# Performance work log

Measured on AMD Instinct MI355X. Metric: run time of the kernel, lower is better.

Reference implementation:

```python
import jax, jax.numpy as jnp
import numpy as np

B, T, C, NH = 8, 1024, 1024, 16
DH = C // NH  # 64


def setup_inputs() -> dict:
    key = jax.random.key(0)
    ks = jax.random.split(key, 7)
    s = 1.0 / np.sqrt(C)
    return {
        "x": jax.random.normal(ks[0], (B, T, C), dtype=jnp.float32),
        "Wq": jax.random.normal(ks[1], (C, C), dtype=jnp.float32) * s,
        "bq": jnp.zeros((C,), dtype=jnp.float32),
        "Wk": jax.random.normal(ks[2], (C, C), dtype=jnp.float32) * s,
        "bk": jnp.zeros((C,), dtype=jnp.float32),
        "Wv": jax.random.normal(ks[3], (C, C), dtype=jnp.float32) * s,
        "bv": jnp.zeros((C,), dtype=jnp.float32),
    }


def reference(x, Wq, bq, Wk, bk, Wv, bv):
    # Linear projections (weights stored as [in, out])
    q = x @ Wq + bq  # [B, T, C]
    k = x @ Wk + bk
    v = x @ Wv + bv
    q = q.reshape(B, T, NH, DH)
    k = k.reshape(B, T, NH, DH)
    v = v.reshape(B, T, NH, DH)
    scale = 1.0 / np.sqrt(DH)
    # NOTE: source module's causal mask buffer is all-ones due to a non-inplace
    # masked_fill bug, so attention is NON-causal (mask multiply is a no-op).
    attn = jnp.einsum("bqhd,bkhd->bhqk", q, k) * scale  # [B, NH, T, T]
    attn = jax.nn.softmax(attn, axis=-1)
    # dropout is identity (p=0 / eval)
    o = jnp.einsum("bhqk,bkhd->bqhd", attn, v)  # [B, T, NH, DH]
    return o.reshape(B, T, C)
```

## Files before the change

kernel.cpp:

```cpp
#include <hip/hip_runtime.h>


#define B_  8
#define T_  1024
#define C_  1024
#define NH_ 16
#define DH_ 64
#define M_  (B_ * T_)

typedef __bf16 bf16x8 __attribute__((ext_vector_type(8)));
typedef float  floatx4 __attribute__((ext_vector_type(4)));

__device__ __forceinline__ unsigned short f2bf(float f) {
    unsigned int u = __float_as_uint(f);
    unsigned int r = (u + 0x7fffu + ((u >> 16) & 1u)) >> 16;
    return (unsigned short)r;
}

__device__ __forceinline__ unsigned int f2bf2(float a, float b) {
    unsigned int ua = __float_as_uint(a), ub = __float_as_uint(b);
    ua += 0x7fffu + ((ua >> 16) & 1u);
    ub += 0x7fffu + ((ub >> 16) & 1u);
#if __has_builtin(__builtin_amdgcn_perm)
    return __builtin_amdgcn_perm(ub, ua, 0x07060302u);
#else
    return (ua >> 16) | (ub & 0xffff0000u);
#endif
}

__device__ __forceinline__ void gload_lds16(const void* g, void* l) {
    __builtin_amdgcn_global_load_lds(
        (const __attribute__((address_space(1))) unsigned int*)g,
        (__attribute__((address_space(3))) unsigned int*)l, 16, 0, 0);
}

__global__ __launch_bounds__(256) void prep_kernel(
    const float* __restrict__ x, unsigned short* __restrict__ xb,
    const float* __restrict__ Wq, const float* __restrict__ Wk,
    const float* __restrict__ Wv, unsigned short* __restrict__ WtAll)
{
    int blk = blockIdx.x;
    if (blk < 8192) {
        int i = blk * 256 + threadIdx.x;
        float4 v = ((const float4*)x)[i];
        ushort4 o;
        unsigned int lo = f2bf2(v.x, v.y), hi = f2bf2(v.z, v.w);
        o.x = (unsigned short)lo; o.y = (unsigned short)(lo >> 16);
        o.z = (unsigned short)hi; o.w = (unsigned short)(hi >> 16);
        ((ushort4*)xb)[i] = o;
        return;
    }
    int tb3 = blk - 8192;
    int which = tb3 >> 8;
    int tb = tb3 & 255;
    const float* W = (which == 0) ? Wq : ((which == 1) ? Wk : Wv);
    unsigned short* out = WtAll + (size_t)which * C_ * C_;

    __shared__ __align__(16) unsigned short tile[64 * 65];
    int k0 = (tb >> 4) * 64, n0 = (tb & 15) * 64;
    int c = threadIdx.x & 63, r0 = threadIdx.x >> 6;

    for (int j = 0; j < 16; ++j) {
        int r = r0 + j * 4;
        tile[c * 65 + r] = f2bf(W[(size_t)(k0 + r) * C_ + n0 + c]);
    }
    __syncthreads();
    for (int j = 0; j < 16; ++j) {
        int r = r0 + j * 4;
        out[(size_t)(n0 + r) * C_ + k0 + c] = tile[r * 65 + c];
    }
}

__global__ __launch_bounds__(256) void qkv_gemm_kernel(
    const unsigned short* __restrict__ xb,
    const unsigned short* __restrict__ WtAll,
    const float* __restrict__ bq, const float* __restrict__ bk,
    const float* __restrict__ bv,
    unsigned short* __restrict__ Qb, unsigned short* __restrict__ Kb,
    unsigned short* __restrict__ Vt)
{
    int which = blockIdx.z;
    const unsigned short* W = WtAll + (size_t)which * C_ * C_;
    const float* bias = (which == 0) ? bq : ((which == 1) ? bk : bv);
    float oscale = (which == 0) ? 0.125f * 1.44269504f : 1.0f;

    __shared__ __align__(16) unsigned short As[128 * 64];
    __shared__ __align__(16) unsigned short Bs[128 * 64];

    int tid = threadIdx.x;
    int wave = tid >> 6, lane = tid & 63;
    int quad = lane >> 4, l16 = lane & 15, l7 = l16 & 7;
    int wm = wave >> 1, wn = wave & 1;
    int bm = blockIdx.x, bn = blockIdx.y;

    floatx4 acc[4][4] = {};

    for (int kk = 0; kk < C_; kk += 64) {
        __syncthreads();
        #pragma unroll
        for (int i = 0; i < 4; ++i) {
            int c = (wave * 4 + i) * 64 + lane;
            int row = c >> 3;
            int lcol = ((c & 7) ^ (row & 7)) * 8;
            gload_lds16(&xb[(size_t)(bm * 128 + row) * C_ + kk + lcol],
                        &As[(wave * 4 + i) * 512]);
            gload_lds16(&W[(size_t)(bn * 128 + row) * C_ + kk + lcol],
                        &Bs[(wave * 4 + i) * 512]);
        }
        __syncthreads();
        #pragma unroll
        for (int s = 0; s < 2; ++s) {
            bf16x8 a[4], bfr[4];
            #pragma unroll
            for (int mt = 0; mt < 4; ++mt) {
                int row = wm * 64 + mt * 16 + l16;
                a[mt] = *(const bf16x8*)&As[row * 64 + ((s * 4 + quad) ^ l7) * 8];
            }
            #pragma unroll
            for (int nt = 0; nt < 4; ++nt) {
                int row = wn * 64 + nt * 16 + l16;
                bfr[nt] = *(const bf16x8*)&Bs[row * 64 + ((s * 4 + quad) ^ l7) * 8];
            }
            if (which < 2) {
                #pragma unroll
                for (int mt = 0; mt < 4; ++mt)
                    #pragma unroll
                    for (int nt = 0; nt < 4; ++nt)
                        acc[mt][nt] = __builtin_amdgcn_mfma_f32_16x16x32_bf16(
                            bfr[nt], a[mt], acc[mt][nt], 0, 0, 0);
            } else {
                #pragma unroll
                for (int mt = 0; mt < 4; ++mt)
                    #pragma unroll
                    for (int nt = 0; nt < 4; ++nt)
                        acc[mt][nt] = __builtin_amdgcn_mfma_f32_16x16x32_bf16(
                            a[mt], bfr[nt], acc[mt][nt], 0, 0, 0);
            }
        }
    }

    if (which < 2) {
        unsigned short* outp = (which == 0) ? Qb : Kb;
        #pragma unroll
        for (int mt = 0; mt < 4; ++mt) {
            int tg = bm * 128 + wm * 64 + mt * 16 + l16;
            int bb = tg >> 10, t = tg & (T_ - 1);
            #pragma unroll
            for (int nt = 0; nt < 4; ++nt) {
                int colg = bn * 128 + wn * 64 + nt * 16 + quad * 4;
                int h = colg >> 6, d = colg & 63;
                float4 b4 = *(const float4*)&bias[colg];
                uint2 o;
                o.x = f2bf2((acc[mt][nt][0] + b4.x) * oscale,
                            (acc[mt][nt][1] + b4.y) * oscale);
                o.y = f2bf2((acc[mt][nt][2] + b4.z) * oscale,
                            (acc[mt][nt][3] + b4.w) * oscale);
                *(uint2*)&outp[((size_t)(bb * NH_ + h) * T_ + t) * DH_ + d] = o;
            }
        }
    } else {
        #pragma unroll
        for (int nt = 0; nt < 4; ++nt) {
            int colg = bn * 128 + wn * 64 + nt * 16 + l16;
            int h = colg >> 6, d = colg & 63;
            float bval = bias[colg];
            #pragma unroll
            for (int mt = 0; mt < 4; ++mt) {
                int tg = bm * 128 + wm * 64 + mt * 16 + quad * 4;
                int bb = tg >> 10, t = tg & (T_ - 1);
                uint2 o;
                o.x = f2bf2(acc[mt][nt][0] + bval, acc[mt][nt][1] + bval);
                o.y = f2bf2(acc[mt][nt][2] + bval, acc[mt][nt][3] + bval);
                *(uint2*)&Vt[((size_t)(bb * NH_ + h) * DH_ + d) * T_ + t] = o;
            }
        }
    }
}

__global__ __launch_bounds__(256) void attn_kernel(
    const unsigned short* __restrict__ Qb,
    const unsigned short* __restrict__ Kb,
    const unsigned short* __restrict__ Vt,
    float* __restrict__ out)
{
    int bh = blockIdx.x;
    int qblk = blockIdx.y;
    int b = bh >> 4, h = bh & (NH_ - 1);
    int tid = threadIdx.x;
    int wave = tid >> 6, lane = tid & 63;
    int quad = lane >> 4, l16 = lane & 15, l7 = l16 & 7;

    const unsigned short* Qh = Qb + (size_t)bh * T_ * DH_;
    const unsigned short* Kh = Kb + (size_t)bh * T_ * DH_;
    const unsigned short* Vh = Vt + (size_t)bh * DH_ * T_;

    __shared__ __align__(16) unsigned short Ks[128 * 64];
    __shared__ __align__(16) unsigned short Vs[64 * 128];
    __shared__ __align__(16) unsigned short Ps[4][2][16 * 72];

    bf16x8 qa[2][2];
    #pragma unroll
    for (int mt = 0; mt < 2; ++mt) {
        int qrow = qblk * 128 + (wave * 2 + mt) * 16 + l16;
        qa[mt][0] = *(const bf16x8*)&Qh[(size_t)qrow * DH_ + quad * 8];
        qa[mt][1] = *(const bf16x8*)&Qh[(size_t)qrow * DH_ + 32 + quad * 8];
    }

    floatx4 o_acc[2][4] = {};
    float l_i[2] = {0.0f, 0.0f};

    for (int kt2 = 0; kt2 < T_ / 128; ++kt2) {
        __syncthreads();
        #pragma unroll
        for (int i = 0; i < 4; ++i) {
            int c = (wave * 4 + i) * 64 + lane;
            int krow = c >> 3;
            int klcol = ((c & 7) ^ (krow & 7)) * 8;
            gload_lds16(&Kh[(size_t)(kt2 * 128 + krow) * DH_ + klcol],
                        &Ks[(wave * 4 + i) * 512]);
            int vrow = c >> 4;
            int vlcol = (((c & 15) ^ (vrow & 15))) * 8;
            gload_lds16(&Vh[(size_t)vrow * T_ + kt2 * 128 + vlcol],
                        &Vs[(wave * 4 + i) * 512]);
        }
        __syncthreads();

        #pragma unroll
        for (int kh = 0; kh < 2; ++kh) {
            floatx4 st[2][4] = {};
            #pragma unroll
            for (int nt = 0; nt < 4; ++nt) {
                int r = (kh * 64 + nt * 16 + l16) * 64;
                bf16x8 k0 = *(const bf16x8*)&Ks[r + ((quad    ) ^ l7) * 8];
                bf16x8 k1 = *(const bf16x8*)&Ks[r + ((quad + 4) ^ l7) * 8];
                #pragma unroll
                for (int mt = 0; mt < 2; ++mt) {
                    st[mt][nt] = __builtin_amdgcn_mfma_f32_16x16x32_bf16(k0, qa[mt][0], st[mt][nt], 0, 0, 0);
                    st[mt][nt] = __builtin_amdgcn_mfma_f32_16x16x32_bf16(k1, qa[mt][1], st[mt][nt], 0, 0, 0);
                }
            }

            #pragma unroll
            for (int mt = 0; mt < 2; ++mt) {
                float rs = 0.0f;
                #pragma unroll
                for (int nt = 0; nt < 4; ++nt) {
                    float e0 = exp2f(st[mt][nt][0]);
                    float e1 = exp2f(st[mt][nt][1]);
                    float e2 = exp2f(st[mt][nt][2]);
                    float e3 = exp2f(st[mt][nt][3]);
                    rs += (e0 + e1) + (e2 + e3);
                    uint2 pk;
                    pk.x = f2bf2(e0, e1);
                    pk.y = f2bf2(e2, e3);
                    *(uint2*)&Ps[wave][mt][l16 * 72 + nt * 16 + quad * 4] = pk;
                }
                rs += __shfl_xor(rs, 16);
                rs += __shfl_xor(rs, 32);
                l_i[mt] += rs;
            }

            #pragma unroll
            for (int s2 = 0; s2 < 2; ++s2) {
                bf16x8 vb[4];
                #pragma unroll
                for (int dt = 0; dt < 4; ++dt) {
                    int chv = (kh * 8 + s2 * 4 + quad) ^ l16;
                    vb[dt] = *(const bf16x8*)&Vs[(dt * 16 + l16) * 128 + chv * 8];
                }
                #pragma unroll
                for (int mt = 0; mt < 2; ++mt) {
                    bf16x8 pb = *(const bf16x8*)&Ps[wave][mt][l16 * 72 + s2 * 32 + quad * 8];
                    #pragma unroll
                    for (int dt = 0; dt < 4; ++dt)
                        o_acc[mt][dt] = __builtin_amdgcn_mfma_f32_16x16x32_bf16(
                            vb[dt], pb, o_acc[mt][dt], 0, 0, 0);
                }
            }
        }
    }

    #pragma unroll
    for (int mt = 0; mt < 2; ++mt) {
        float inv = 1.0f / l_i[mt];
        int t = qblk * 128 + (wave * 2 + mt) * 16 + l16;
        float* op = &out[((size_t)b * T_ + t) * C_ + h * DH_];
        #pragma unroll
        for (int dt = 0; dt < 4; ++dt) {
            float4 v;
            v.x = o_acc[mt][dt][0] * inv;
            v.y = o_acc[mt][dt][1] * inv;
            v.z = o_acc[mt][dt][2] * inv;
            v.w = o_acc[mt][dt][3] * inv;
            *(float4*)&op[dt * 16 + quad * 4] = v;
        }
    }
}

extern "C" void kernel_launch(void* const* d_in, const int* in_sizes, int n_in,
                              void* d_out, int out_size, void* d_ws, size_t ws_size,
                              hipStream_t stream) {
    const float* x  = (const float*)d_in[0];
    const float* Wq = (const float*)d_in[1];
    const float* bq = (const float*)d_in[2];
    const float* Wk = (const float*)d_in[3];
    const float* bk = (const float*)d_in[4];
    const float* Wv = (const float*)d_in[5];
    const float* bv = (const float*)d_in[6];
    float* out = (float*)d_out;

    char* ws = (char*)d_ws;
    size_t off = 0;
    unsigned short* xb = (unsigned short*)(ws + off); off += (size_t)M_ * C_ * 2;
    unsigned short* Wt = (unsigned short*)(ws + off); off += (size_t)3 * C_ * C_ * 2;
    unsigned short* Qb = (unsigned short*)(ws + off); off += (size_t)M_ * C_ * 2;
    unsigned short* Kb = (unsigned short*)(ws + off); off += (size_t)M_ * C_ * 2;
    unsigned short* Vt = (unsigned short*)(ws + off); off += (size_t)M_ * C_ * 2;

    prep_kernel<<<dim3(8960), dim3(256), 0, stream>>>(x, xb, Wq, Wk, Wv, Wt);

    qkv_gemm_kernel<<<dim3(M_ / 128, C_ / 128, 3), dim3(256), 0, stream>>>(
        xb, Wt, bq, bk, bv, Qb, Kb, Vt);

    attn_kernel<<<dim3(B_ * NH_, T_ / 128), dim3(256), 0, stream>>>(Qb, Kb, Vt, out);
}
```

Measured before the change: 233.3 us.

## Switch attention to 32x32x16 MFMA with register-resident P and vectorized weight transpose

Rewrites the attention inner loops to use 32x32x16 bf16 MFMA tiles. The softmax probabilities now stay in registers, exchanged between lane halves with cross-lane shuffles, so the per-wave LDS staging buffer and its round trip are gone. Launch bounds now request 4 blocks per SM. The weight-transpose prep kernel also switches to a padded tile with 4-element vector stores. The aim is fewer LDS accesses and higher MFMA efficiency, at the cost of more register pressure and shuffle work.

```diff
diff --git a/kernel.cpp b/kernel.cpp
--- a/kernel.cpp
+++ b/kernel.cpp
@@ -10,6 +10,8 @@
 
 typedef __bf16 bf16x8 __attribute__((ext_vector_type(8)));
 typedef float  floatx4 __attribute__((ext_vector_type(4)));
+typedef float  floatx16 __attribute__((ext_vector_type(16)));
+typedef unsigned int uintx4 __attribute__((ext_vector_type(4)));
 
 __device__ __forceinline__ unsigned short f2bf(float f) {
     unsigned int u = __float_as_uint(f);
@@ -56,18 +58,21 @@
     const float* W = (which == 0) ? Wq : ((which == 1) ? Wk : Wv);
     unsigned short* out = WtAll + (size_t)which * C_ * C_;
 
-    __shared__ __align__(16) unsigned short tile[64 * 65];
+    __shared__ __align__(16) unsigned short tile[64 * 68];
     int k0 = (tb >> 4) * 64, n0 = (tb & 15) * 64;
     int c = threadIdx.x & 63, r0 = threadIdx.x >> 6;
 
     for (int j = 0; j < 16; ++j) {
         int r = r0 + j * 4;
-        tile[c * 65 + r] = f2bf(W[(size_t)(k0 + r) * C_ + n0 + c]);
+        tile[c * 68 + r] = f2bf(W[(size_t)(k0 + r) * C_ + n0 + c]);
     }
     __syncthreads();
-    for (int j = 0; j < 16; ++j) {
-        int r = r0 + j * 4;
-        out[(size_t)(n0 + r) * C_ + k0 + c] = tile[r * 65 + c];
+    int k4 = (threadIdx.x & 15) * 4;
+    int nw = threadIdx.x >> 4;
+    for (int it = 0; it < 4; ++it) {
+        int n = nw + it * 16;
+        ushort4 o = *(const ushort4*)&tile[n * 68 + k4];
+        *(ushort4*)&out[(size_t)(n0 + n) * C_ + k0 + k4] = o;
     }
 }
 
@@ -177,7 +182,7 @@
     }
 }
 
-__global__ __launch_bounds__(256) void attn_kernel(
+__global__ __launch_bounds__(256, 4) void attn_kernel(
     const unsigned short* __restrict__ Qb,
     const unsigned short* __restrict__ Kb,
     const unsigned short* __restrict__ Vt,
@@ -188,7 +193,7 @@
     int b = bh >> 4, h = bh & (NH_ - 1);
     int tid = threadIdx.x;
     int wave = tid >> 6, lane = tid & 63;
-    int quad = lane >> 4, l16 = lane & 15, l7 = l16 & 7;
+    int l5 = lane & 31, hi = lane >> 5;
 
     const unsigned short* Qh = Qb + (size_t)bh * T_ * DH_;
     const unsigned short* Kh = Kb + (size_t)bh * T_ * DH_;
@@ -196,18 +201,15 @@
 
     __shared__ __align__(16) unsigned short Ks[128 * 64];
     __shared__ __align__(16) unsigned short Vs[64 * 128];
-    __shared__ __align__(16) unsigned short Ps[4][2][16 * 72];
-
-    bf16x8 qa[2][2];
+
+    int qrow = qblk * 128 + wave * 32 + l5;
+    bf16x8 qa[4];
     #pragma unroll
-    for (int mt = 0; mt < 2; ++mt) {
-        int qrow = qblk * 128 + (wave * 2 + mt) * 16 + l16;
-        qa[mt][0] = *(const bf16x8*)&Qh[(size_t)qrow * DH_ + quad * 8];
-        qa[mt][1] = *(const bf16x8*)&Qh[(size_t)qrow * DH_ + 32 + quad * 8];
-    }
-
-    floatx4 o_acc[2][4] = {};
-    float l_i[2] = {0.0f, 0.0f};
+    for (int sl = 0; sl < 4; ++sl)
+        qa[sl] = *(const bf16x8*)&Qh[(size_t)qrow * DH_ + sl * 16 + hi * 8];
+
+    floatx16 o_acc[2] = {};
+    float l_i = 0.0f;
 
     for (int kt2 = 0; kt2 < T_ / 128; ++kt2) {
         __syncthreads();
@@ -219,7 +221,7 @@
             gload_lds16(&Kh[(size_t)(kt2 * 128 + krow) * DH_ + klcol],
                         &Ks[(wave * 4 + i) * 512]);
             int vrow = c >> 4;
-            int vlcol = (((c & 15) ^ (vrow & 15))) * 8;
+            int vlcol = ((c & 15) ^ (vrow & 15)) * 8;
             gload_lds16(&Vh[(size_t)vrow * T_ + kt2 * 128 + vlcol],
                         &Vs[(wave * 4 + i) * 512]);
         }
@@ -227,72 +229,77 @@
 
         #pragma unroll
         for (int kh = 0; kh < 2; ++kh) {
-            floatx4 st[2][4] = {};
-            #pragma unroll
-            for (int nt = 0; nt < 4; ++nt) {
-                int r = (kh * 64 + nt * 16 + l16) * 64;
-                bf16x8 k0 = *(const bf16x8*)&Ks[r + ((quad    ) ^ l7) * 8];
-                bf16x8 k1 = *(const bf16x8*)&Ks[r + ((quad + 4) ^ l7) * 8];
-                #pragma unroll
-                for (int mt = 0; mt < 2; ++mt) {
-                    st[mt][nt] = __builtin_amdgcn_mfma_f32_16x16x32_bf16(k0, qa[mt][0], st[mt][nt], 0, 0, 0);
-                    st[mt][nt] = __builtin_amdgcn_mfma_f32_16x16x32_bf16(k1, qa[mt][1], st[mt][nt], 0, 0, 0);
+            floatx16 st[2] = {};
+            #pragma unroll
+            for (int nt = 0; nt < 2; ++nt) {
+                int r = kh * 64 + nt * 32 + l5;
+                #pragma unroll
+                for (int sl = 0; sl < 4; ++sl) {
+                    bf16x8 kb = *(const bf16x8*)&Ks[r * 64 + (((sl * 2 + hi)) ^ (r & 7)) * 8];
+                    st[nt] = __builtin_amdgcn_mfma_f32_32x32x16_bf16(
+                        kb, qa[sl], st[nt], 0, 0, 0);
                 }
             }
 
-            #pragma unroll
-            for (int mt = 0; mt < 2; ++mt) {
+            unsigned int pd[2][8];
+            #pragma unroll
+            for (int nt = 0; nt < 2; ++nt) {
                 float rs = 0.0f;
                 #pragma unroll
-                for (int nt = 0; nt < 4; ++nt) {
-                    float e0 = exp2f(st[mt][nt][0]);
-                    float e1 = exp2f(st[mt][nt][1]);
-                    float e2 = exp2f(st[mt][nt][2]);
-                    float e3 = exp2f(st[mt][nt][3]);
-                    rs += (e0 + e1) + (e2 + e3);
-                    uint2 pk;
-                    pk.x = f2bf2(e0, e1);
-                    pk.y = f2bf2(e2, e3);
-                    *(uint2*)&Ps[wave][mt][l16 * 72 + nt * 16 + quad * 4] = pk;
+                for (int m = 0; m < 8; ++m) {
+                    float e0 = exp2f(st[nt][2 * m]);
+                    float e1 = exp2f(st[nt][2 * m + 1]);
+                    rs += e0 + e1;
+                    pd[nt][m] = f2bf2(e0, e1);
                 }
-                rs += __shfl_xor(rs, 16);
-                rs += __shfl_xor(rs, 32);
-                l_i[mt] += rs;
-            }
-
-            #pragma unroll
-            for (int s2 = 0; s2 < 2; ++s2) {
-                bf16x8 vb[4];
-                #pragma unroll
-                for (int dt = 0; dt < 4; ++dt) {
-                    int chv = (kh * 8 + s2 * 4 + quad) ^ l16;
-                    vb[dt] = *(const bf16x8*)&Vs[(dt * 16 + l16) * 128 + chv * 8];
+                l_i += rs;
+            }
+
+            #pragma unroll
+            for (int ks = 0; ks < 4; ++ks) {
+                int nt = ks >> 1, base = (ks & 1) * 4;
+                uintx4 pbu;
+                {
+                    unsigned int c0 = pd[nt][base + 0], c2 = pd[nt][base + 2];
+                    unsigned int uk = hi ? c2 : c0;
+                    unsigned int us = hi ? c0 : c2;
+                    unsigned int rr = (unsigned int)__shfl_xor((int)us, 32);
+                    pbu.x = hi ? rr : uk;
+                    pbu.z = hi ? uk : rr;
+                    unsigned int c1 = pd[nt][base + 1], c3 = pd[nt][base + 3];
+                    uk = hi ? c3 : c1;
+                    us = hi ? c1 : c3;
+                    rr = (unsigned int)__shfl_xor((int)us, 32);
+                    pbu.y = hi ? rr : uk;
+                    pbu.w = hi ? uk : rr;
                 }
-                #pragma unroll
-                for (int mt = 0; mt < 2; ++mt) {
-                    bf16x8 pb = *(const bf16x8*)&Ps[wave][mt][l16 * 72 + s2 * 32 + quad * 8];
-                    #pragma unroll
-                    for (int dt = 0; dt < 4; ++dt)
-                        o_acc[mt][dt] = __builtin_amdgcn_mfma_f32_16x16x32_bf16(
-                            vb[dt], pb, o_acc[mt][dt], 0, 0, 0);
+                bf16x8 pb = __builtin_bit_cast(bf16x8, pbu);
+                int ch = (kh * 4 + ks) * 2 + hi;
+                #pragma unroll
+                for (int dt = 0; dt < 2; ++dt) {
+                    int vr = dt * 32 + l5;
+                    bf16x8 vb = *(const bf16x8*)&Vs[vr * 128 + (ch ^ (vr & 15)) * 8];
+                    o_acc[dt] = __builtin_amdgcn_mfma_f32_32x32x16_bf16(
+                        vb, pb, o_acc[dt], 0, 0, 0);
                 }
             }
         }
     }
 
+    float lt = l_i + __shfl_xor(l_i, 32);
+    float inv = 1.0f / lt;
+    int t = qblk * 128 + wave * 32 + l5;
+    float* op = &out[((size_t)b * T_ + t) * C_ + h * DH_];
     #pragma unroll
-    for (int mt = 0; mt < 2; ++mt) {
-        float inv = 1.0f / l_i[mt];
-        int t = qblk * 128 + (wave * 2 + mt) * 16 + l16;
-        float* op = &out[((size_t)b * T_ + t) * C_ + h * DH_];
-        #pragma unroll
-        for (int dt = 0; dt < 4; ++dt) {
+    for (int dt = 0; dt < 2; ++dt) {
+        #pragma unroll
+        for (int g = 0; g < 4; ++g) {
             float4 v;
-            v.x = o_acc[mt][dt][0] * inv;
-            v.y = o_acc[mt][dt][1] * inv;
-            v.z = o_acc[mt][dt][2] * inv;
-            v.w = o_acc[mt][dt][3] * inv;
-            *(float4*)&op[dt * 16 + quad * 4] = v;
+            v.x = o_acc[dt][g * 4 + 0] * inv;
+            v.y = o_acc[dt][g * 4 + 1] * inv;
+            v.z = o_acc[dt][g * 4 + 2] * inv;
+            v.w = o_acc[dt][g * 4 + 3] * inv;
+            *(float4*)&op[dt * 32 + g * 8 + hi * 4] = v;
         }
     }
 }
```

After: 261.2 us. +12.0%, slower.
